# Performance work log

Measured on AMD Instinct MI355X. Metric: run time of the kernel, lower is better.

The kernel has to match this reference:

```python
import jax, jax.numpy as jnp
import numpy as np
import math

EMB_ATOM = 256
PAIR_IN = 64
PAIR_OUT = 64
EMB_RBF = 16
N_ATOMS = 50000
N_EDGES = 1_600_000
KMAX = 32


def setup_inputs() -> dict:
    key = jax.random.key(0)
    ks = jax.random.split(key, 8)
    h = jax.random.normal(ks[0], (N_ATOMS, EMB_ATOM), dtype=jnp.float32)
    rad_basis = jax.random.normal(ks[1], (N_ATOMS, EMB_RBF, KMAX), dtype=jnp.float32)
    edge_index = jax.random.randint(ks[2], (2, N_EDGES), 0, N_ATOMS, dtype=jnp.int64)
    target_neighbor_idx = jax.random.randint(ks[3], (N_EDGES,), 0, KMAX, dtype=jnp.int64)
    # Learned parameters (Dense layers are bias-free); stored as [in, out].
    W_down = jax.random.normal(ks[4], (EMB_ATOM, PAIR_IN), dtype=jnp.float32) / math.sqrt(EMB_ATOM)
    W_bilinear = jax.random.normal(ks[5], (EMB_RBF * PAIR_IN, PAIR_OUT), dtype=jnp.float32) / math.sqrt(EMB_RBF * PAIR_IN)
    W_up = jax.random.normal(ks[6], (PAIR_OUT, EMB_ATOM), dtype=jnp.float32) / math.sqrt(PAIR_OUT)
    scale = jnp.ones((), dtype=jnp.float32)  # ScaleFactor learned scalar
    return {"h": h, "rad_basis": rad_basis, "edge_index": edge_index,
            "target_neighbor_idx": target_neighbor_idx, "W_down": W_down,
            "W_bilinear": W_bilinear, "W_up": W_up, "scale": scale}


def reference(h, rad_basis, edge_index, target_neighbor_idx, W_down, W_bilinear, W_up, scale):
    num_atoms = h.shape[0]
    kmax = rad_basis.shape[-1]
    pair_in = W_down.shape[-1]
    # down_projection (Dense, silu activation, no bias)
    x_b = jax.nn.silu(h @ W_down)                              # [N, pair_in]
    x_ba = x_b[edge_index[0]]                                  # [E, pair_in] gather by source atom
    # scatter edge features into padded per-atom neighbor buffer
    x2 = jnp.zeros((num_atoms, kmax, pair_in), dtype=x_ba.dtype)
    x2 = x2.at[edge_index[1], target_neighbor_idx].set(x_ba)   # [N, Kmax, pair_in]
    # rbf-weighted neighbor aggregation: batched matmul
    x_ba2 = jnp.einsum('nrk,nkd->nrd', rad_basis, x2)          # [N, rbf, pair_in]
    h_out = x_ba2.reshape(num_atoms, -1) @ W_bilinear          # bilinear Dense, no activation
    h_out = h_out * scale                                      # ScaleFactor
    return jax.nn.silu(h_out @ W_up)                           # up_projection
```

## Files before the change

kernel.cpp:

```cpp
#include <hip/hip_runtime.h>

typedef __attribute__((ext_vector_type(8))) short short8;
typedef __attribute__((ext_vector_type(4))) float floatx4;
typedef unsigned short u16;
typedef unsigned int u32;
typedef unsigned long long u64;

#define KMAXN 32

__device__ __forceinline__ u16 f2b(float f) {
    unsigned u = __builtin_bit_cast(unsigned, f);
    u += 0x7FFFu + ((u >> 16) & 1u);
    return (u16)(u >> 16);
}
__device__ __forceinline__ float silu_f(float x) {
    return x / (1.f + __expf(-x));
}

__global__ __launch_bounds__(256) void k_init(const float* __restrict__ Wd,
                                              const float* __restrict__ Wb,
                                              const float* __restrict__ Wu,
                                              u16* __restrict__ WdT,
                                              u16* __restrict__ WbT2,
                                              u16* __restrict__ WuT,
                                              u64* __restrict__ win64,
                                              u16* __restrict__ xb,
                                              int nslots) {
    long idx = (long)blockIdx.x * 256 + threadIdx.x;
    if (idx < 16384) {
        WdT[idx] = f2b(Wd[(idx & 255) * 64 + (idx >> 8)]);
    } else if (idx < 81920) {
        int i = (int)idx - 16384;
        int n = i >> 10, s = i & 1023;
        int d = s >> 4, rbf = s & 15;
        WbT2[i] = f2b(Wb[(rbf * 64 + d) * 64 + n]);
    } else if (idx < 98304) {
        int i = (int)idx - 81920;
        WuT[i] = f2b(Wu[(i & 63) * 256 + (i >> 6)]);
    } else {
        long z = idx - 98304;
        uint4 zero = {0, 0, 0, 0};
        if (z < nslots / 2) {
            reinterpret_cast<uint4*>(win64)[z] = zero;
            if (z < 8) {
                long N = nslots / KMAXN;
                reinterpret_cast<uint4*>(xb + N * 64)[z] = zero;
            }
        }
    }
}

__global__ __launch_bounds__(256) void k_prep(const float* __restrict__ h,
                                              const u16*   __restrict__ WdT,
                                              u16*         __restrict__ xb,
                                              const int*   __restrict__ esrc,
                                              const int*   __restrict__ edst,
                                              const int*   __restrict__ tni,
                                              u64*         __restrict__ win64,
                                              int E, int DOWN) {
    const int tid = threadIdx.x;
    if ((int)blockIdx.x >= DOWN) {
        int e = (blockIdx.x - DOWN) * 256 + tid;
        if (e < E) {
            u64 v = ((u64)(unsigned)(e + 1) << 32) | (u32)esrc[e];
            atomicMax(&win64[(long)edst[e] * KMAXN + tni[e]], v);
        }
        return;
    }
    const int wave = tid >> 6;
    const int lane = tid & 63;
    const int m = lane & 15;
    const int q = lane >> 4;
    const long atom0 = (long)blockIdx.x * 16;

    const float* arow = h + (atom0 + m) * 256 + q * 8;
    const u16* brow = WdT + (wave * 16 + m) * 256 + q * 8;
    floatx4 acc = {0.f, 0.f, 0.f, 0.f};
#pragma unroll
    for (int kk = 0; kk < 8; ++kk) {
        float4 f0 = *reinterpret_cast<const float4*>(arow + kk * 32);
        float4 f1 = *reinterpret_cast<const float4*>(arow + kk * 32 + 4);
        short8 a;
        a[0] = (short)f2b(f0.x); a[1] = (short)f2b(f0.y);
        a[2] = (short)f2b(f0.z); a[3] = (short)f2b(f0.w);
        a[4] = (short)f2b(f1.x); a[5] = (short)f2b(f1.y);
        a[6] = (short)f2b(f1.z); a[7] = (short)f2b(f1.w);
        short8 b = *reinterpret_cast<const short8*>(brow + kk * 32);
        acc = __builtin_amdgcn_mfma_f32_16x16x32_bf16(a, b, acc, 0, 0, 0);
    }
#pragma unroll
    for (int r = 0; r < 4; ++r) {
        xb[(atom0 + q * 4 + r) * 64 + wave * 16 + m] = f2b(silu_f(acc[r]));
    }
}

#define T_STRIDE 1032

__global__ __launch_bounds__(256, 2) void k_fused(
        const float* __restrict__ rad,
        const u16*   __restrict__ xb,
        const u64*   __restrict__ win64,
        const u16*   __restrict__ WbT2,
        const u16*   __restrict__ WuT,
        const float* __restrict__ scale_p,
        float* __restrict__ out,
        int N) {
    __shared__ alignas(16) u16 t2[16][T_STRIDE];
    __shared__ alignas(16) u16 c2_lds[16][72];

    const int tid  = threadIdx.x;
    const int wave = tid >> 6;
    const int lane = tid & 63;
    const int m = lane & 15;
    const int q = lane >> 4;
    const long atom0 = (long)blockIdx.x * 16;
    const long nbase = atom0 + wave * 4;

    uint4 w[4][4];
#pragma unroll
    for (int a = 0; a < 4; ++a) {
        const uint4* wp = reinterpret_cast<const uint4*>(win64 + (nbase + a) * KMAXN + q * 8);
#pragma unroll
        for (int i = 0; i < 4; ++i) w[a][i] = wp[i];
    }
    float4 rf[4][2];
#pragma unroll
    for (int a = 0; a < 4; ++a) {
        const float* rrow = rad + (nbase + a) * 512 + m * 32 + q * 8;
        rf[a][0] = *reinterpret_cast<const float4*>(rrow);
        rf[a][1] = *reinterpret_cast<const float4*>(rrow + 4);
    }
    u32 off[4][8];
#pragma unroll
    for (int a = 0; a < 4; ++a) {
        off[a][0] = (w[a][0].y ? w[a][0].x : (u32)N) * 64u + (u32)m;
        off[a][1] = (w[a][0].w ? w[a][0].z : (u32)N) * 64u + (u32)m;
        off[a][2] = (w[a][1].y ? w[a][1].x : (u32)N) * 64u + (u32)m;
        off[a][3] = (w[a][1].w ? w[a][1].z : (u32)N) * 64u + (u32)m;
        off[a][4] = (w[a][2].y ? w[a][2].x : (u32)N) * 64u + (u32)m;
        off[a][5] = (w[a][2].w ? w[a][2].z : (u32)N) * 64u + (u32)m;
        off[a][6] = (w[a][3].y ? w[a][3].x : (u32)N) * 64u + (u32)m;
        off[a][7] = (w[a][3].w ? w[a][3].z : (u32)N) * 64u + (u32)m;
    }
    u32 gv[4][8][4];
#pragma unroll
    for (int a = 0; a < 4; ++a) {
#pragma unroll
        for (int j = 0; j < 8; ++j) {
            const u16* p = xb + off[a][j];
#pragma unroll
            for (int c = 0; c < 4; ++c) {
                gv[a][j][c] = (u32)p[c * 16];
            }
        }
    }
    short8 ra[4];
#pragma unroll
    for (int a = 0; a < 4; ++a) {
        ra[a][0] = (short)f2b(rf[a][0].x); ra[a][1] = (short)f2b(rf[a][0].y);
        ra[a][2] = (short)f2b(rf[a][0].z); ra[a][3] = (short)f2b(rf[a][0].w);
        ra[a][4] = (short)f2b(rf[a][1].x); ra[a][5] = (short)f2b(rf[a][1].y);
        ra[a][6] = (short)f2b(rf[a][1].z); ra[a][7] = (short)f2b(rf[a][1].w);
    }

#pragma unroll
    for (int a = 0; a < 4; ++a) {
#pragma unroll
        for (int c = 0; c < 4; ++c) {
            union { u32 u[4]; short8 s; } bx;
            bx.u[0] = (gv[a][0][c] & 0xffffu) | (gv[a][1][c] << 16);
            bx.u[1] = (gv[a][2][c] & 0xffffu) | (gv[a][3][c] << 16);
            bx.u[2] = (gv[a][4][c] & 0xffffu) | (gv[a][5][c] << 16);
            bx.u[3] = (gv[a][6][c] & 0xffffu) | (gv[a][7][c] << 16);
            floatx4 tz = {0.f, 0.f, 0.f, 0.f};
            tz = __builtin_amdgcn_mfma_f32_16x16x32_bf16(ra[a], bx.s, tz, 0, 0, 0);
            u32 lo = (u32)f2b(tz[0]) | ((u32)f2b(tz[1]) << 16);
            u32 hi = (u32)f2b(tz[2]) | ((u32)f2b(tz[3]) << 16);
            u64 val = (u64)lo | ((u64)hi << 32);
            *reinterpret_cast<u64*>(&t2[wave * 4 + a][(c * 16 + m) * 16 + q * 4]) = val;
        }
    }
    __syncthreads();

    floatx4 c2 = {0.f, 0.f, 0.f, 0.f};
    const u16* wbrow = WbT2 + (wave * 16 + m) * 1024 + q * 8;
#pragma unroll 4
    for (int kk = 0; kk < 32; ++kk) {
        short8 af = *reinterpret_cast<const short8*>(&t2[m][kk * 32 + q * 8]);
        short8 bf = *reinterpret_cast<const short8*>(wbrow + kk * 32);
        c2 = __builtin_amdgcn_mfma_f32_16x16x32_bf16(af, bf, c2, 0, 0, 0);
    }
    {
        float sc = scale_p[0];
#pragma unroll
        for (int r = 0; r < 4; ++r) {
            c2_lds[q * 4 + r][wave * 16 + m] = f2b(c2[r] * sc);
        }
    }
    __syncthreads();

#pragma unroll
    for (int tt = 0; tt < 4; ++tt) {
        floatx4 acc = {0.f, 0.f, 0.f, 0.f};
        const u16* wurow = WuT + (wave * 64 + tt * 16 + m) * 64 + q * 8;
#pragma unroll
        for (int ks = 0; ks < 2; ++ks) {
            short8 af = *reinterpret_cast<const short8*>(&c2_lds[m][ks * 32 + q * 8]);
            short8 bf = *reinterpret_cast<const short8*>(wurow + ks * 32);
            acc = __builtin_amdgcn_mfma_f32_16x16x32_bf16(af, bf, acc, 0, 0, 0);
        }
#pragma unroll
        for (int r = 0; r < 4; ++r) {
            out[(atom0 + q * 4 + r) * 256 + wave * 64 + tt * 16 + m] = silu_f(acc[r]);
        }
    }
}

extern "C" void kernel_launch(void* const* d_in, const int* in_sizes, int n_in,
                              void* d_out, int out_size, void* d_ws, size_t ws_size,
                              hipStream_t stream) {
    const float* h     = (const float*)d_in[0];
    const float* rad   = (const float*)d_in[1];
    const int*   eidx  = (const int*)d_in[2];
    const int*   tni   = (const int*)d_in[3];
    const float* Wd    = (const float*)d_in[4];
    const float* Wb    = (const float*)d_in[5];
    const float* Wu    = (const float*)d_in[6];
    const float* scale = (const float*)d_in[7];
    float* out         = (float*)d_out;

    const int E = in_sizes[3];
    const int N = in_sizes[0] / 256;
    const int nslots = N * KMAXN;

    u16* xb = (u16*)d_ws;
    size_t off = (size_t)(N + 1) * 64 * sizeof(u16);
    u64* win64 = (u64*)((char*)d_ws + off);
    off += (size_t)nslots * sizeof(u64);
    u16* WdT  = (u16*)((char*)d_ws + off);  off += 16384 * 2;
    u16* WbT2 = (u16*)((char*)d_ws + off);  off += 65536 * 2;
    u16* WuT  = (u16*)((char*)d_ws + off);

    const int DOWN = N / 16;
    const int WIN  = (E + 255) / 256;
    const int INIT = 384 + (nslots / 2 + 255) / 256;

    k_init<<<INIT, 256, 0, stream>>>(Wd, Wb, Wu, WdT, WbT2, WuT, win64, xb, nslots);
    k_prep<<<DOWN + WIN, 256, 0, stream>>>(h, WdT, xb, eidx, eidx + E, tni, win64, E, DOWN);
    k_fused<<<DOWN, 256, 0, stream>>>(rad, xb, win64, WbT2, WuT, scale, out, N);
}
```

Measured before the change: 356.0 us.

## Replicate 32-bit winner table across copies and merge before fused kernel

The 64-bit atomicMax over (edge id, source) per neighbor slot is replaced by a 32-bit atomicMax on edge id only, spread across up to 8 replicated tables chosen by block index to reduce atomic contention. A new merge kernel reduces the replicas, resolves the winning edge's source atom (or the padding row), and writes a compact 32-bit source table that the fused kernel reads directly. This halves the per-slot width the fused kernel loads, but costs a larger zero-init and an extra kernel launch with one pass over all replicas.

```diff
diff --git a/kernel.cpp b/kernel.cpp
--- a/kernel.cpp
+++ b/kernel.cpp
@@ -23,9 +23,9 @@
                                               u16* __restrict__ WdT,
                                               u16* __restrict__ WbT2,
                                               u16* __restrict__ WuT,
-                                              u64* __restrict__ win64,
+                                              u32* __restrict__ win32,
                                               u16* __restrict__ xb,
-                                              int nslots) {
+                                              int nslots, int nt) {
     long idx = (long)blockIdx.x * 256 + threadIdx.x;
     if (idx < 16384) {
         WdT[idx] = f2b(Wd[(idx & 255) * 64 + (idx >> 8)]);
@@ -39,9 +39,10 @@
         WuT[i] = f2b(Wu[(i & 63) * 256 + (i >> 6)]);
     } else {
         long z = idx - 98304;
+        long ztot = (long)nt * nslots / 4;
         uint4 zero = {0, 0, 0, 0};
-        if (z < nslots / 2) {
-            reinterpret_cast<uint4*>(win64)[z] = zero;
+        if (z < ztot) {
+            reinterpret_cast<uint4*>(win32)[z] = zero;
             if (z < 8) {
                 long N = nslots / KMAXN;
                 reinterpret_cast<uint4*>(xb + N * 64)[z] = zero;
@@ -56,14 +57,15 @@
                                               const int*   __restrict__ esrc,
                                               const int*   __restrict__ edst,
                                               const int*   __restrict__ tni,
-                                              u64*         __restrict__ win64,
-                                              int E, int DOWN) {
+                                              u32*         __restrict__ win32,
+                                              int E, int DOWN, int nslots, int tmask) {
     const int tid = threadIdx.x;
     if ((int)blockIdx.x >= DOWN) {
-        int e = (blockIdx.x - DOWN) * 256 + tid;
+        int wb = blockIdx.x - DOWN;
+        int e = wb * 256 + tid;
         if (e < E) {
-            u64 v = ((u64)(unsigned)(e + 1) << 32) | (u32)esrc[e];
-            atomicMax(&win64[(long)edst[e] * KMAXN + tni[e]], v);
+            size_t tbase = (size_t)(wb & tmask) * nslots;
+            atomicMax(&win32[tbase + (size_t)edst[e] * KMAXN + tni[e]], (u32)(e + 1));
         }
         return;
     }
@@ -94,17 +96,29 @@
     }
 }
 
+__global__ __launch_bounds__(256) void k_merge(u32* __restrict__ win32,
+                                               const int* __restrict__ esrc,
+                                               int nslots, int nt, int N) {
+    int s = blockIdx.x * 256 + threadIdx.x;
+    if (s >= nslots) return;
+    u32 w = win32[s];
+    for (int t = 1; t < nt; ++t) {
+        u32 v = win32[(size_t)t * nslots + s];
+        w = v > w ? v : w;
+    }
+    win32[s] = w ? (u32)esrc[w - 1] : (u32)N;
+}
+
 #define T_STRIDE 1032
 
 __global__ __launch_bounds__(256, 2) void k_fused(
         const float* __restrict__ rad,
         const u16*   __restrict__ xb,
-        const u64*   __restrict__ win64,
+        const u32*   __restrict__ src32,
         const u16*   __restrict__ WbT2,
         const u16*   __restrict__ WuT,
         const float* __restrict__ scale_p,
-        float* __restrict__ out,
-        int N) {
+        float* __restrict__ out) {
     __shared__ alignas(16) u16 t2[16][T_STRIDE];
     __shared__ alignas(16) u16 c2_lds[16][72];
 
@@ -116,12 +130,12 @@
     const long atom0 = (long)blockIdx.x * 16;
     const long nbase = atom0 + wave * 4;
 
-    uint4 w[4][4];
-#pragma unroll
-    for (int a = 0; a < 4; ++a) {
-        const uint4* wp = reinterpret_cast<const uint4*>(win64 + (nbase + a) * KMAXN + q * 8);
-#pragma unroll
-        for (int i = 0; i < 4; ++i) w[a][i] = wp[i];
+    uint4 sv[4][2];
+#pragma unroll
+    for (int a = 0; a < 4; ++a) {
+        const uint4* sp = reinterpret_cast<const uint4*>(src32 + (nbase + a) * KMAXN + q * 8);
+        sv[a][0] = sp[0];
+        sv[a][1] = sp[1];
     }
     float4 rf[4][2];
 #pragma unroll
@@ -133,14 +147,14 @@
     u32 off[4][8];
 #pragma unroll
     for (int a = 0; a < 4; ++a) {
-        off[a][0] = (w[a][0].y ? w[a][0].x : (u32)N) * 64u + (u32)m;
-        off[a][1] = (w[a][0].w ? w[a][0].z : (u32)N) * 64u + (u32)m;
-        off[a][2] = (w[a][1].y ? w[a][1].x : (u32)N) * 64u + (u32)m;
-        off[a][3] = (w[a][1].w ? w[a][1].z : (u32)N) * 64u + (u32)m;
-        off[a][4] = (w[a][2].y ? w[a][2].x : (u32)N) * 64u + (u32)m;
-        off[a][5] = (w[a][2].w ? w[a][2].z : (u32)N) * 64u + (u32)m;
-        off[a][6] = (w[a][3].y ? w[a][3].x : (u32)N) * 64u + (u32)m;
-        off[a][7] = (w[a][3].w ? w[a][3].z : (u32)N) * 64u + (u32)m;
+        off[a][0] = sv[a][0].x * 64u + (u32)m;
+        off[a][1] = sv[a][0].y * 64u + (u32)m;
+        off[a][2] = sv[a][0].z * 64u + (u32)m;
+        off[a][3] = sv[a][0].w * 64u + (u32)m;
+        off[a][4] = sv[a][1].x * 64u + (u32)m;
+        off[a][5] = sv[a][1].y * 64u + (u32)m;
+        off[a][6] = sv[a][1].z * 64u + (u32)m;
+        off[a][7] = sv[a][1].w * 64u + (u32)m;
     }
     u32 gv[4][8][4];
 #pragma unroll
@@ -233,19 +247,27 @@
     const int N = in_sizes[0] / 256;
     const int nslots = N * KMAXN;
 
+    const size_t xb_bytes = (size_t)(N + 1) * 64 * sizeof(u16);
+    const size_t w_bytes  = (16384 + 65536 + 16384) * sizeof(u16);
+    size_t need8 = xb_bytes + (size_t)8 * nslots * sizeof(u32) + w_bytes;
+    const int NT = (ws_size >= need8) ? 8 : 1;
+
     u16* xb = (u16*)d_ws;
-    size_t off = (size_t)(N + 1) * 64 * sizeof(u16);
-    u64* win64 = (u64*)((char*)d_ws + off);
-    off += (size_t)nslots * sizeof(u64);
+    size_t off = xb_bytes;
+    u32* win32 = (u32*)((char*)d_ws + off);
+    off += (size_t)NT * nslots * sizeof(u32);
     u16* WdT  = (u16*)((char*)d_ws + off);  off += 16384 * 2;
     u16* WbT2 = (u16*)((char*)d_ws + off);  off += 65536 * 2;
     u16* WuT  = (u16*)((char*)d_ws + off);
 
     const int DOWN = N / 16;
     const int WIN  = (E + 255) / 256;
-    const int INIT = 384 + (nslots / 2 + 255) / 256;
-
-    k_init<<<INIT, 256, 0, stream>>>(Wd, Wb, Wu, WdT, WbT2, WuT, win64, xb, nslots);
-    k_prep<<<DOWN + WIN, 256, 0, stream>>>(h, WdT, xb, eidx, eidx + E, tni, win64, E, DOWN);
-    k_fused<<<DOWN, 256, 0, stream>>>(rad, xb, win64, WbT2, WuT, scale, out, N);
-}
+    const int INIT = 384 + ((long)NT * nslots / 4 + 255) / 256;
+    const int MERGE = (nslots + 255) / 256;
+
+    k_init<<<INIT, 256, 0, stream>>>(Wd, Wb, Wu, WdT, WbT2, WuT, win32, xb, nslots, NT);
+    k_prep<<<DOWN + WIN, 256, 0, stream>>>(h, WdT, xb, eidx, eidx + E, tni, win32,
+                                           E, DOWN, nslots, NT - 1);
+    k_merge<<<MERGE, 256, 0, stream>>>(win32, eidx, nslots, NT, N);
+    k_fused<<<DOWN, 256, 0, stream>>>(rad, xb, win32, WbT2, WuT, scale, out);
+}
```

Result: slower. 378.4 us (+6.3%).
